# Optimization experiments

Measured on AMD Instinct MI355X. Metric: run time of the kernel, lower is better.

Reference implementation:

```python
import jax, jax.numpy as jnp
import numpy as np

T, B, IN, H, L = 1024, 128, 100, 200, 2


def _lstm_layer(x, h0, c0, W_ih, W_hh, b_ih, b_hh):
    # x: [T, B, in]; h0, c0: [B, H]; W_ih: [4H, in]; W_hh: [4H, H]
    # PyTorch gate order: i, f, g, o
    def step(carry, x_t):
        h, c = carry
        gates = x_t @ W_ih.T + b_ih + h @ W_hh.T + b_hh  # [B, 4H]
        i, f, g, o = jnp.split(gates, 4, axis=-1)
        i = jax.nn.sigmoid(i)
        f = jax.nn.sigmoid(f)
        g = jnp.tanh(g)
        o = jax.nn.sigmoid(o)
        c = f * c + i * g
        h = o * jnp.tanh(c)
        return (h, c), h

    (hT, cT), ys = jax.lax.scan(step, (h0, c0), x)
    return ys, hT, cT  # ys: [T, B, H]


def setup_inputs() -> dict:
    key = jax.random.key(0)
    ks = jax.random.split(key, 12)
    s = 1.0 / np.sqrt(H)  # PyTorch LSTM init scale
    return {
        "inp": jax.random.normal(ks[0], (T, B, IN), dtype=jnp.float32),
        "h0": jnp.zeros((L, B, H), dtype=jnp.float32),
        "c0": jnp.zeros((L, B, H), dtype=jnp.float32),
        "W_ih0": jax.random.uniform(ks[1], (4 * H, IN), jnp.float32, -s, s),
        "W_hh0": jax.random.uniform(ks[2], (4 * H, H), jnp.float32, -s, s),
        "b_ih0": jax.random.uniform(ks[3], (4 * H,), jnp.float32, -s, s),
        "b_hh0": jax.random.uniform(ks[4], (4 * H,), jnp.float32, -s, s),
        "W_ih1": jax.random.uniform(ks[5], (4 * H, H), jnp.float32, -s, s),
        "W_hh1": jax.random.uniform(ks[6], (4 * H, H), jnp.float32, -s, s),
        "b_ih1": jax.random.uniform(ks[7], (4 * H,), jnp.float32, -s, s),
        "b_hh1": jax.random.uniform(ks[8], (4 * H,), jnp.float32, -s, s),
        "fc_W": jax.random.uniform(ks[9], (IN, H), jnp.float32, -s, s),
        "fc_b": jax.random.uniform(ks[10], (IN,), jnp.float32, -s, s),
    }


def reference(inp, h0, c0, W_ih0, W_hh0, b_ih0, b_hh0, W_ih1, W_hh1, b_ih1, b_hh1, fc_W, fc_b):
    # 2-layer LSTM (eval mode: inter-layer dropout is identity) + linear head
    y0, h0T, c0T = _lstm_layer(inp, h0[0], c0[0], W_ih0, W_hh0, b_ih0, b_hh0)
    y1, h1T, c1T = _lstm_layer(y0, h0[1], c0[1], W_ih1, W_hh1, b_ih1, b_hh1)
    output = y1 @ fc_W.T + fc_b  # [T, B, num_classes]
    hn = jnp.stack([h0T, h1T], axis=0)  # [2, B, H]
    cn = jnp.stack([c0T, c1T], axis=0)
    return output, hn, cn
```

## Files before the change

### kernel.cpp

```cpp
#include <hip/hip_runtime.h>
#include <stdint.h>

#define T_ 1024
#define B_ 128
#define IN_ 100
#define H_ 200
#define RD 32
#define RDY 32

typedef unsigned short u16;
typedef unsigned long long u64;
typedef short bf16x8 __attribute__((ext_vector_type(8)));
typedef float f32x4  __attribute__((ext_vector_type(4)));

#define OFF_Y1    0u
#define OFF_Y0R   52428800u
#define OFF_PR0   55705600u
#define OFF_PR1A  68812800u
#define OFF_PR1B  81920000u
#define OFF_PACK  95027200u
#define OFF_CBF   96358400u
#define OFF_CH0   97525056u
#define OFF_CC0   97729856u
#define OFF_FLG   97934656u
#define WS_NEEDED 97938816u
#define FO_X0P  0u
#define FO_Y0P  512u
#define FO_W1A  1024u
#define FO_W1B  1536u
#define FO_WY0A 2048u
#define FO_WY0B 2560u
#define FO_CN0  3072u
#define FO_CN1  3584u
#define FO_DTF  4096u
#define PK_WHH0 0
#define PK_WHH1 179200
#define PK_WIH0 358400
#define PK_WIH1 460800

__device__ __forceinline__ float bf2f(u16 u) {
    union { uint32_t i; float f; } v; v.i = ((uint32_t)u) << 16; return v.f;
}
__device__ __forceinline__ u16 f2bf(float f) {
    union { uint32_t i; float f; } v; v.f = f;
    uint32_t x = v.i;
    x += 0x7fff + ((x >> 16) & 1);
    return (u16)(x >> 16);
}
__device__ __forceinline__ void agst2(float* p, float a, float b) {
    union { u64 u; float f[2]; } v; v.f[0] = a; v.f[1] = b;
    __hip_atomic_store((u64*)p, v.u, __ATOMIC_RELAXED, __HIP_MEMORY_SCOPE_AGENT);
}
__device__ __forceinline__ float2 agld2(const float* p) {
    union { u64 u; float f[2]; } v;
    v.u = __hip_atomic_load((u64*)p, __ATOMIC_RELAXED, __HIP_MEMORY_SCOPE_AGENT);
    return make_float2(v.f[0], v.f[1]);
}
__device__ __forceinline__ void agsti(int* p, int v) {
    __hip_atomic_store(p, v, __ATOMIC_RELAXED, __HIP_MEMORY_SCOPE_AGENT);
}
__device__ __forceinline__ void spin_ge(int* p, int val, int* budget) {
    while (__hip_atomic_load(p, __ATOMIC_RELAXED, __HIP_MEMORY_SCOPE_AGENT) < val) {
        __builtin_amdgcn_s_sleep(1);
        if (--(*budget) < 0) return;
    }
}
__device__ __forceinline__ float fsig(float x) {
    const float e = __expf(-x);
    return __builtin_amdgcn_rcpf(1.f + e);
}
__device__ __forceinline__ float ftanh(float x) {
    const float ax = __builtin_fabsf(x);
    const float e = __expf(-2.f * ax);
    const float r = (1.f - e) * __builtin_amdgcn_rcpf(1.f + e);
    return __builtin_copysignf(r, x);
}

__global__ void detect_kernel(const void* w, int* flag) {
    __shared__ int cnt;
    if (threadIdx.x == 0) cnt = 0;
    __syncthreads();
    const u16* p = (const u16*)w;
    int bad = 0;
    for (int e = 0; e < 16; ++e) {
        u16 u = p[threadIdx.x * 16 + e];
        int ex = (u >> 7) & 0xFF;
        float v = bf2f(u);
        float av = v < 0.f ? -v : v;
        if (ex == 0xFF || av > 0.5f) bad++;
    }
    atomicAdd(&cnt, bad);
    __syncthreads();
    if (threadIdx.x == 0) flag[0] = (cnt > 64) ? 1 : 0;
}

__global__ void prep_kernel(const void* Wih0, const void* Whh0,
                            const void* bih0, const void* bhh0,
                            const void* Wih1, const void* Whh1,
                            const void* bih1, const void* bhh1,
                            const void* fcW,  const void* fcb,
                            const void* h0,   const void* c0,
                            u16* cbf, float* ch0, float* cc0, const int* flag)
{
    const int isf32 = *flag;
    const int N = 685700;
    for (int idx = blockIdx.x * 256 + threadIdx.x; idx < N; idx += gridDim.x * 256) {
        const void* src; int e = idx; u16* du = nullptr; float* df = nullptr;
        if (e < 80000)                 { src = Wih0; du = cbf; }
        else if ((e -= 80000) < 160000){ src = Whh0; du = cbf + 80000; }
        else if ((e -= 160000) < 800)  { src = bih0; du = cbf + 240000; }
        else if ((e -= 800) < 800)     { src = bhh0; du = cbf + 240800; }
        else if ((e -= 800) < 160000)  { src = Wih1; du = cbf + 241600; }
        else if ((e -= 160000) < 160000){ src = Whh1; du = cbf + 401600; }
        else if ((e -= 160000) < 800)  { src = bih1; du = cbf + 561600; }
        else if ((e -= 800) < 800)     { src = bhh1; du = cbf + 562400; }
        else if ((e -= 800) < 20000)   { src = fcW;  du = cbf + 563200; }
        else if ((e -= 20000) < 100)   { src = fcb;  du = cbf + 583200; }
        else if ((e -= 100) < 51200)   { src = h0;   df = ch0; }
        else         { e -= 51200;       src = c0;   df = cc0; }
        float v = isf32 ? ((const float*)src)[e] : bf2f(((const u16*)src)[e]);
        if (du) du[e] = f2bf(v); else df[e] = v;
    }
}

__global__ void pack_kernel(const u16* __restrict__ cbf, u16* __restrict__ pw) {
    const int N = 665600;
    for (int idx = blockIdx.x * 256 + threadIdx.x; idx < N; idx += gridDim.x * 256) {
        int e = idx; const u16* src; int ld, koff, kmax, rel;
        if (e < 179200)                    { rel = e; src = cbf + 80000;  ld = 200; kmax = 200; koff = 0; }
        else if ((e -= 179200) < 179200)   { rel = e; src = cbf + 401600; ld = 200; kmax = 200; koff = 0; }
        else if ((e -= 179200) < 102400)   { rel = e; src = cbf + 0;      ld = 100; kmax = 100; koff = 0; }
        else { e -= 102400; const int kh = e / 102400; rel = e % 102400;
               src = cbf + 241600; ld = 200; kmax = 100; koff = kh * 100; }
        const int el = rel & 7, l = (rel >> 3) & 63, tile = rel >> 9;
        const int nt = tile % 50, kt = tile / 50;
        const int rp = nt * 16 + (l & 15), g = rp & 3, hc = rp >> 2;
        const int k = kt * 32 + ((l >> 4) << 3) + el;
        u16 v = 0;
        if (k < kmax) v = src[(g * 200 + hc) * ld + koff + k];
        pw[idx] = v;
    }
}

__launch_bounds__(512, 1)
__global__ void lstm_pipe(const void* __restrict__ inp, char* __restrict__ ws,
                          const int* __restrict__ flag, void* __restrict__ out)
{
    __shared__ __align__(16) u16 smem[67392];

    u16*   y1buf  = (u16*)(ws + OFF_Y1);
    float* y0ring = (float*)(ws + OFF_Y0R);
    float* pr0    = (float*)(ws + OFF_PR0);
    float* pr1a   = (float*)(ws + OFF_PR1A);
    float* pr1b   = (float*)(ws + OFF_PR1B);
    u16*   packs  = (u16*)(ws + OFF_PACK);
    const u16* cbf = (const u16*)(ws + OFF_CBF);
    const float* ch0 = (const float*)(ws + OFF_CH0);
    const float* cc0 = (const float*)(ws + OFF_CC0);

    const int isf32 = *flag;
    const int tid = threadIdx.x;
    const int bid = blockIdx.x;
    const int lane = tid & 63, wv = tid >> 6;
    const int lm = lane & 15, lq = lane >> 4;
    const int nslot = (wv < 2) ? 7 : 6;
    int budget = 1 << 22;

    if (bid < 16) {
        const int L = bid >> 3, i = bid & 7, b0 = i * 16;
        const int FI = i * 16;
        int* fx0p = (int*)(ws + OFF_FLG + FO_X0P) + FI;
        int* fw1a = (int*)(ws + OFF_FLG + FO_W1A) + FI;
        int* fw1b = (int*)(ws + OFF_FLG + FO_W1B) + FI;
        int* fwy0a= (int*)(ws + OFF_FLG + FO_WY0A) + FI;
        int* fwy0b= (int*)(ws + OFF_FLG + FO_WY0B) + FI;
        int* fy0p = (int*)(ws + OFF_FLG + FO_Y0P) + FI;
        int* fcn0 = (int*)(ws + OFF_FLG + FO_CN0) + FI;
        int* fcn1 = (int*)(ws + OFF_FLG + FO_CN1) + FI;

        u16* ldsB = smem;
        u16* hls  = smem + 31744;
        float* gls = (float*)(smem + 40192);
        const u16* packW = packs + (L ? PK_WHH1 : PK_WHH0);

        bf16x8 Bv[36];
        #pragma unroll
        for (int s = 0; s < 7; ++s) {
            const int nt = (s < 6) ? (wv + 8 * s) : (48 + wv);
            #pragma unroll
            for (int kt = 0; kt < 7; ++kt) {
                if (s < 5) {
                    Bv[s * 7 + kt] = *(const bf16x8*)(packW + ((size_t)(kt * 50 + nt) * 64 + lane) * 8);
                } else if (s == 5 && kt == 0) {
                    Bv[35] = *(const bf16x8*)(packW + ((size_t)(kt * 50 + nt) * 64 + lane) * 8);
                }
            }
        }
        for (int u = tid; u < 31744; u += 512) {
            const int eidx = u >> 9, off = u & 511;
            int kt, nt;
            if (eidx < 48) { kt = 1 + eidx % 6; nt = (eidx / 6) + 40; }
            else { const int e2 = eidx - 48; kt = e2 % 7; nt = 48 + e2 / 7; }
            ldsB[u] = packW[(size_t)(kt * 50 + nt) * 512 + off];
        }
        for (int u = tid; u < 2 * 16 * 264; u += 512) {
            const int pl = u / (16 * 264), m = (u / 264) % 16, k = u % 264;
            u16 v = 0;
            if (k < 200) {
                const float h = ch0[L * B_ * H_ + (b0 + m) * H_ + k];
                const u16 hi = f2bf(h);
                v = pl ? f2bf(h - bf2f(hi)) : hi;
            }
            hls[u] = v;
        }
        float c2[4][2];
        #pragma unroll
        for (int k4 = 0; k4 < 4; ++k4) {
            const int p = tid + 512 * k4;
            c2[k4][0] = 0.f; c2[k4][1] = 0.f;
            if (p < 1600) {
                const int m = p / 100, hc = (p % 100) * 2;
                c2[k4][0] = cc0[L * B_ * H_ + (b0 + m) * H_ + hc];
                c2[k4][1] = cc0[L * B_ * H_ + (b0 + m) * H_ + hc + 1];
            }
        }
        f32x4 acc[7];
        if (tid == 0) {
            if (L == 0) spin_ge(fx0p, 1, &budget);
            else        { spin_ge(fw1a, 1, &budget); spin_ge(fw1b, 1, &budget); }
        }
        __syncthreads();
        {
            const size_t roff = (size_t)(0 * 8 + i) * 12800;
            #pragma unroll
            for (int s = 0; s < 7; ++s) if (s < nslot) {
                const int nt = (s < 6) ? (wv + 8 * s) : (48 + wv);
                float* pa = ((L ? pr1a : pr0) + roff) + nt * 256 + lane * 4;
                const float2 a01 = agld2(pa);
                const float2 a23 = agld2(pa + 2);
                acc[s][0] = a01.x; acc[s][1] = a01.y;
                acc[s][2] = a23.x; acc[s][3] = a23.y;
                if (L) {
                    float* pb = (pr1b + roff) + nt * 256 + lane * 4;
                    const float2 b01 = agld2(pb);
                    const float2 b23 = agld2(pb + 2);
                    acc[s][0] += b01.x; acc[s][1] += b01.y;
                    acc[s][2] += b23.x; acc[s][3] += b23.y;
                }
            }
        }
        __syncthreads();

        for (int t = 0; t < T_; ++t) {
            #pragma unroll
            for (int kt = 0; kt < 7; ++kt) {
                const int ha = lm * 264 + kt * 32 + 8 * lq;
                const bf16x8 Ahi = *(const bf16x8*)(hls + ha);
                const bf16x8 Alo = *(const bf16x8*)(hls + 16 * 264 + ha);
                #pragma unroll
                for (int s = 0; s < 7; ++s) if (s < nslot) {
                    bf16x8 Bt;
                    if (s < 5)                 Bt = Bv[s * 7 + kt];
                    else if (s == 5 && kt == 0) Bt = Bv[35];
                    else {
                        const int eidx = (s == 5) ? (wv * 6 + kt - 1) : (48 + wv * 7 + kt);
                        Bt = *(const bf16x8*)(ldsB + eidx * 512 + lane * 8);
                    }
                    acc[s] = __builtin_amdgcn_mfma_f32_16x16x32_bf16(Ahi, Bt, acc[s], 0, 0, 0);
                    acc[s] = __builtin_amdgcn_mfma_f32_16x16x32_bf16(Alo, Bt, acc[s], 0, 0, 0);
                }
            }
            #pragma unroll
            for (int s = 0; s < 7; ++s) if (s < nslot) {
                const int nt = (s < 6) ? (wv + 8 * s) : (48 + wv);
                const int g = lm & 3, hc = nt * 4 + (lm >> 2);
                float* gp = gls + g * 3400 + hc * 17 + 4 * lq;
                gp[0] = acc[s][0]; gp[1] = acc[s][1]; gp[2] = acc[s][2]; gp[3] = acc[s][3];
            }
            __syncthreads();
            if ((t & 7) == 0) {
                if (tid == 0) {
                    int tgt = t + 9; if (tgt > T_) tgt = T_;
                    if (L == 0) {
                        spin_ge(fx0p, tgt, &budget);
                        spin_ge(fwy0a, t - 15, &budget);
                        spin_ge(fwy0b, t - 15, &budget);
                    } else {
                        spin_ge(fw1a, tgt, &budget);
                        spin_ge(fw1b, tgt, &budget);
                    }
                }
                __syncthreads();
            }
            if (t < T_ - 1) {
                const size_t roff = (size_t)(((t + 1) & (RD - 1)) * 8 + i) * 12800;
                #pragma unroll
                for (int s = 0; s < 7; ++s) if (s < nslot) {
                    const int nt = (s < 6) ? (wv + 8 * s) : (48 + wv);
                    float* pa = ((L ? pr1a : pr0) + roff) + nt * 256 + lane * 4;
                    const float2 a01 = agld2(pa);
                    const float2 a23 = agld2(pa + 2);
                    acc[s][0] = a01.x; acc[s][1] = a01.y;
                    acc[s][2] = a23.x; acc[s][3] = a23.y;
                    if (L) {
                        float* pb = (pr1b + roff) + nt * 256 + lane * 4;
                        const float2 b01 = agld2(pb);
                        const float2 b23 = agld2(pb + 2);
                        acc[s][0] += b01.x; acc[s][1] += b01.y;
                        acc[s][2] += b23.x; acc[s][3] += b23.y;
                    }
                }
            }
            #pragma unroll
            for (int k4 = 0; k4 < 4; ++k4) {
                const int p = tid + 512 * k4;
                if (p < 1600) {
                    const int m = p / 100, hc = (p % 100) * 2;
                    float ig0 = gls[hc * 17 + m],        ig1 = gls[(hc + 1) * 17 + m];
                    float fg0 = gls[3400 + hc * 17 + m], fg1 = gls[3400 + (hc + 1) * 17 + m];
                    float gg0 = gls[6800 + hc * 17 + m], gg1 = gls[6800 + (hc + 1) * 17 + m];
                    float og0 = gls[10200 + hc * 17 + m],og1 = gls[10200 + (hc + 1) * 17 + m];
                    ig0 = (ig0 == ig0) ? ig0 : 0.f;  ig1 = (ig1 == ig1) ? ig1 : 0.f;
                    fg0 = (fg0 == fg0) ? fg0 : 0.f;  fg1 = (fg1 == fg1) ? fg1 : 0.f;
                    gg0 = (gg0 == gg0) ? gg0 : 0.f;  gg1 = (gg1 == gg1) ? gg1 : 0.f;
                    og0 = (og0 == og0) ? og0 : 0.f;  og1 = (og1 == og1) ? og1 : 0.f;
                    ig0 = fsig(ig0); ig1 = fsig(ig1);
                    fg0 = fsig(fg0); fg1 = fsig(fg1);
                    og0 = fsig(og0); og1 = fsig(og1);
                    gg0 = ftanh(gg0); gg1 = ftanh(gg1);
                    c2[k4][0] = fg0 * c2[k4][0] + ig0 * gg0;
                    c2[k4][1] = fg1 * c2[k4][1] + ig1 * gg1;
                    const float h0v = og0 * ftanh(c2[k4][0]);
                    const float h1v = og1 * ftanh(c2[k4][1]);
                    const u16 hi0 = f2bf(h0v), hi1 = f2bf(h1v);
                    const u16 lo0 = f2bf(h0v - bf2f(hi0)), lo1 = f2bf(h1v - bf2f(hi1));
                    *(uint32_t*)(hls + m * 264 + hc) = (uint32_t)hi0 | ((uint32_t)hi1 << 16);
                    *(uint32_t*)(hls + (16 + m) * 264 + hc) = (uint32_t)lo0 | ((uint32_t)lo1 << 16);
                    if (L == 0) {
                        agst2(y0ring + ((size_t)(t & (RDY - 1)) * B_ + b0 + m) * H_ + hc, h0v, h1v);
                    } else {
                        *(uint32_t*)(y1buf + ((size_t)t * B_ + b0 + m) * H_ + hc)
                            = (uint32_t)hi0 | ((uint32_t)hi1 << 16);
                    }
                    if (t == T_ - 1) {
                        const size_t base = (size_t)T_ * B_ * IN_;
                        const size_t bb = (size_t)(b0 + m) * H_ + hc;
                        const size_t o1 = base + (size_t)L * B_ * H_ + bb;
                        const size_t o2 = base + 2 * (size_t)B_ * H_ + (size_t)L * B_ * H_ + bb;
                        if (isf32) {
                            ((float*)out)[o1] = h0v; ((float*)out)[o1 + 1] = h1v;
                            ((float*)out)[o2] = c2[k4][0]; ((float*)out)[o2 + 1] = c2[k4][1];
                        } else {
                            ((u16*)out)[o1] = hi0; ((u16*)out)[o1 + 1] = hi1;
                            ((u16*)out)[o2] = f2bf(c2[k4][0]); ((u16*)out)[o2 + 1] = f2bf(c2[k4][1]);
                        }
                    }
                }
            }
            __syncthreads();
            if (tid == 0) {
                if (L == 0) {
                    agsti(fy0p, t + 1);
                    if (((t + 1) & 7) == 0) agsti(fcn0, t + 1);
                } else {
                    if (((t + 1) & 7) == 0) agsti(fcn1, t + 1);
                }
            }
        }
    } else {
        const int isx0 = (bid < 24);
        const int i  = isx0 ? (bid - 16) : ((bid - 24) >> 1);
        const int kh = isx0 ? 0 : ((bid - 24) & 1);
        const int b0 = i * 16;
        const int FI = i * 16;
        int* fx0p = (int*)(ws + OFF_FLG + FO_X0P) + FI;
        int* fy0p = (int*)(ws + OFF_FLG + FO_Y0P) + FI;
        int* fw1  = (int*)(ws + OFF_FLG + (kh ? FO_W1B : FO_W1A)) + FI;
        int* fwy0 = (int*)(ws + OFF_FLG + (kh ? FO_WY0B : FO_WY0A)) + FI;
        int* fcons= (int*)(ws + OFF_FLG + (isx0 ? FO_CN0 : FO_CN1)) + FI;

        u16* xst = smem;
        const u16* packW = packs + (isx0 ? PK_WIH0 : (PK_WIH1 + kh * 102400));

        bf16x8 Bx[28];
        #pragma unroll
        for (int s = 0; s < 7; ++s) {
            const int nt = (s < 6) ? (wv + 8 * s) : (48 + wv);
            #pragma unroll
            for (int kt = 0; kt < 4; ++kt)
                if (s < nslot)
                    Bx[s * 4 + kt] = *(const bf16x8*)(packW + ((size_t)(kt * 50 + nt) * 64 + lane) * 8);
        }
        float bias[7];
        #pragma unroll
        for (int s = 0; s < 7; ++s) {
            bias[s] = 0.f;
            if (s < nslot && (isx0 || kh == 0)) {
                const int nt = (s < 6) ? (wv + 8 * s) : (48 + wv);
                const int rp = nt * 16 + lm, g = rp & 3, hc = rp >> 2, R = g * 200 + hc;
                bias[s] = isx0 ? (bf2f(cbf[240000 + R]) + bf2f(cbf[240800 + R]))
                               : (bf2f(cbf[561600 + R]) + bf2f(cbf[562400 + R]));
            }
        }
        for (int u = tid; u < 8704; u += 512) xst[u] = 0;

        float2 sreg[2];
        if (!isx0) { if (tid == 0) spin_ge(fy0p, 1, &budget); }
        __syncthreads();
        #pragma unroll
        for (int j = 0; j < 2; ++j) {
            const int u = tid + 512 * j;
            if (u < 800) {
                const int m = u / 50, k = (u % 50) * 2;
                if (isx0) {
                    const size_t gi = ((size_t)0 * B_ + b0 + m) * IN_ + k;
                    if (isf32) sreg[j] = *(const float2*)((const float*)inp + gi);
                    else { const uint32_t xv = *(const uint32_t*)((const u16*)inp + gi);
                           sreg[j] = make_float2(bf2f((u16)xv), bf2f((u16)(xv >> 16))); }
                } else {
                    sreg[j] = agld2(y0ring + ((size_t)0 * B_ + b0 + m) * H_ + kh * 100 + k);
                }
                const u16 h0 = f2bf(sreg[j].x), h1 = f2bf(sreg[j].y);
                *(uint32_t*)(xst + m * 136 + k) = (uint32_t)h0 | ((uint32_t)h1 << 16);
                *(uint32_t*)(xst + 2176 + m * 136 + k)
                    = (uint32_t)f2bf(sreg[j].x - bf2f(h0)) | ((uint32_t)f2bf(sreg[j].y - bf2f(h1)) << 16);
            }
        }
        __syncthreads();
        int cur = 0;

        for (int t = 0; t < T_; ++t) {
            if (t < T_ - 1) {
                if (tid == 0) {
                    if (isx0) {
                        if ((t & 7) == 0) spin_ge(fcons, t - 23, &budget);
                    } else {
                        spin_ge(fy0p, t + 2, &budget);
                        if ((t & 7) == 0) spin_ge(fcons, t - 23, &budget);
                    }
                }
                __syncthreads();
                #pragma unroll
                for (int j = 0; j < 2; ++j) {
                    const int u = tid + 512 * j;
                    if (u < 800) {
                        const int m = u / 50, k = (u % 50) * 2;
                        if (isx0) {
                            const size_t gi = ((size_t)(t + 1) * B_ + b0 + m) * IN_ + k;
                            if (isf32) sreg[j] = *(const float2*)((const float*)inp + gi);
                            else { const uint32_t xv = *(const uint32_t*)((const u16*)inp + gi);
                                   sreg[j] = make_float2(bf2f((u16)xv), bf2f((u16)(xv >> 16))); }
                        } else {
                            sreg[j] = agld2(y0ring + ((size_t)((t + 1) & (RDY - 1)) * B_ + b0 + m) * H_ + kh * 100 + k);
                        }
                    }
                }
            }
            f32x4 acc[7];
            #pragma unroll
            for (int s = 0; s < 7; ++s) {
                acc[s][0] = bias[s]; acc[s][1] = bias[s];
                acc[s][2] = bias[s]; acc[s][3] = bias[s];
            }
            #pragma unroll
            for (int kt = 0; kt < 4; ++kt) {
                const int xa = cur * 4352 + lm * 136 + kt * 32 + 8 * lq;
                const bf16x8 Ahi = *(const bf16x8*)(xst + xa);
                const bf16x8 Alo = *(const bf16x8*)(xst + 2176 + xa);
                #pragma unroll
                for (int s = 0; s < 7; ++s) if (s < nslot) {
                    acc[s] = __builtin_amdgcn_mfma_f32_16x16x32_bf16(Ahi, Bx[s * 4 + kt], acc[s], 0, 0, 0);
                    acc[s] = __builtin_amdgcn_mfma_f32_16x16x32_bf16(Alo, Bx[s * 4 + kt], acc[s], 0, 0, 0);
                }
            }
            float* ring = (isx0 ? pr0 : (kh ? pr1b : pr1a))
                        + (size_t)((t & (RD - 1)) * 8 + i) * 12800;
            #pragma unroll
            for (int s = 0; s < 7; ++s) if (s < nslot) {
                const int nt = (s < 6) ? (wv + 8 * s) : (48 + wv);
                float* pp = ring + nt * 256 + lane * 4;
                agst2(pp, acc[s][0], acc[s][1]);
                agst2(pp + 2, acc[s][2], acc[s][3]);
            }
            __syncthreads();
            if (tid == 0) {
                if (isx0) { if (((t + 1) & 3) == 0) agsti(fx0p, t + 1); }
                else      { agsti(fw1, t + 1); agsti(fwy0, t + 1); }
            }
            if (t < T_ - 1) {
                const int nb = (cur ^ 1) * 4352;
                #pragma unroll
                for (int j = 0; j < 2; ++j) {
                    const int u = tid + 512 * j;
                    if (u < 800) {
                        const int m = u / 50, k = (u % 50) * 2;
                        const u16 h0 = f2bf(sreg[j].x), h1 = f2bf(sreg[j].y);
                        *(uint32_t*)(xst + nb + m * 136 + k) = (uint32_t)h0 | ((uint32_t)h1 << 16);
                        *(uint32_t*)(xst + nb + 2176 + m * 136 + k)
                            = (uint32_t)f2bf(sreg[j].x - bf2f(h0)) | ((uint32_t)f2bf(sreg[j].y - bf2f(h1)) << 16);
                    }
                }
                __syncthreads();
                cur ^= 1;
            }
        }
    }
}

__launch_bounds__(256)
__global__ void fc_kernel(const u16* __restrict__ y1, const u16* __restrict__ cbf,
                          const int* __restrict__ flag, void* __restrict__ out)
{
    __shared__ float y1s[16 * 201];
    const int isf32 = *flag;
    const u16* fcW = cbf + 563200;
    const u16* fcb = cbf + 583200;
    const int tid = threadIdx.x;
    const int m0 = blockIdx.x * 16;
    for (int idx = tid; idx < 16 * 200; idx += 256) {
        int r = idx / 200, k = idx % 200;
        y1s[r * 201 + k] = bf2f(y1[(size_t)(m0 + r) * 200 + k]);
    }
    __syncthreads();
    const int r = tid & 15, ct = tid >> 4;
    float acc[7] = {0.f, 0.f, 0.f, 0.f, 0.f, 0.f, 0.f};
    for (int k = 0; k < 200; ++k) {
        const float x = y1s[r * 201 + k];
        #pragma unroll
        for (int qn = 0; qn < 7; ++qn) {
            int cc = ct + 16 * qn;
            if (cc < 100) acc[qn] = fmaf(x, bf2f(fcW[cc * 200 + k]), acc[qn]);
        }
    }
    #pragma unroll
    for (int qn = 0; qn < 7; ++qn) {
        int cc = ct + 16 * qn;
        if (cc < 100) {
            float v = acc[qn] + bf2f(fcb[cc]);
            v = (v == v) ? v : 0.f;
            const size_t oi = (size_t)(m0 + r) * 100 + cc;
            if (isf32) ((float*)out)[oi] = v;
            else       ((u16*)out)[oi] = f2bf(v);
        }
    }
}

extern "C" void kernel_launch(void* const* d_in, const int* in_sizes, int n_in,
                              void* d_out, int out_size, void* d_ws, size_t ws_size,
                              hipStream_t stream)
{
    const void* inp  = d_in[0];
    const void* h0   = d_in[1];
    const void* c0   = d_in[2];
    const void* Wih0 = d_in[3];
    const void* Whh0 = d_in[4];
    const void* bih0 = d_in[5];
    const void* bhh0 = d_in[6];
    const void* Wih1 = d_in[7];
    const void* Whh1 = d_in[8];
    const void* bih1 = d_in[9];
    const void* bhh1 = d_in[10];
    const void* fcW  = d_in[11];
    const void* fcb  = d_in[12];

    if (ws_size < WS_NEEDED) return;

    char* ws = (char*)d_ws;
    u16*   cbf  = (u16*)(ws + OFF_CBF);
    float* ch0  = (float*)(ws + OFF_CH0);
    float* cc0  = (float*)(ws + OFF_CC0);
    u16*   pw   = (u16*)(ws + OFF_PACK);
    int*   dflag= (int*)(ws + OFF_FLG + FO_DTF);
    u16*   y1buf= (u16*)(ws + OFF_Y1);

    hipMemsetAsync(ws + OFF_FLG, 0, 4160, stream);

    detect_kernel<<<1, 256, 0, stream>>>(Wih0, dflag);
    prep_kernel<<<512, 256, 0, stream>>>(Wih0, Whh0, bih0, bhh0,
                                         Wih1, Whh1, bih1, bhh1,
                                         fcW, fcb, h0, c0, cbf, ch0, cc0, dflag);
    pack_kernel<<<256, 256, 0, stream>>>(cbf, pw);
    lstm_pipe<<<40, 512, 0, stream>>>(inp, ws, dflag, d_out);
    fc_kernel<<<8192, 256, 0, stream>>>(y1buf, cbf, dflag, d_out);
}
```

Before: 6.453 ms.

## Compute LSTM cell in registers via DPP transposes and double-buffer hidden state

Gate pre-activations are no longer staged through an LDS gate buffer followed by a block-wide barrier. Each lane now uses two DPP quad permutes to gather the four gates (i, f, g, o) for one hidden unit straight from the MFMA accumulators and updates its cell state in registers. The hidden-state LDS buffer is double-buffered so the new h can be written while the current step's A operand is being read, which removes one __syncthreads per timestep and shrinks LDS use. The cost is more permute work, scalar stores in place of paired stores to the y0 ring and y1 buffer, and a layout whose correctness depends on the MFMA output mapping.

New measurement: 7.132 ms. 1.11x slower.

```diff
diff --git a/kernel.cpp b/kernel.cpp
--- a/kernel.cpp
+++ b/kernel.cpp
@@ -51,6 +51,9 @@
     union { u64 u; float f[2]; } v; v.f[0] = a; v.f[1] = b;
     __hip_atomic_store((u64*)p, v.u, __ATOMIC_RELAXED, __HIP_MEMORY_SCOPE_AGENT);
 }
+__device__ __forceinline__ void agst1(float* p, float a) {
+    __hip_atomic_store(p, a, __ATOMIC_RELAXED, __HIP_MEMORY_SCOPE_AGENT);
+}
 __device__ __forceinline__ float2 agld2(const float* p) {
     union { u64 u; float f[2]; } v;
     v.u = __hip_atomic_load((u64*)p, __ATOMIC_RELAXED, __HIP_MEMORY_SCOPE_AGENT);
@@ -75,6 +78,15 @@
     const float r = (1.f - e) * __builtin_amdgcn_rcpf(1.f + e);
     return __builtin_copysignf(r, x);
 }
+template<int CTRL>
+__device__ __forceinline__ float qperm(float x) {
+    union { float f; int i; } u, r;
+    u.f = x;
+    r.i = __builtin_amdgcn_update_dpp(0, u.i, CTRL, 0xF, 0xF, true);
+    return r.f;
+}
+#define QP_XOR1 177
+#define QP_XOR2 78
 
 __global__ void detect_kernel(const void* w, int* flag) {
     __shared__ int cnt;
@@ -146,7 +158,7 @@
 __global__ void lstm_pipe(const void* __restrict__ inp, char* __restrict__ ws,
                           const int* __restrict__ flag, void* __restrict__ out)
 {
-    __shared__ __align__(16) u16 smem[67392];
+    __shared__ __align__(16) u16 smem[48640];
 
     u16*   y1buf  = (u16*)(ws + OFF_Y1);
     float* y0ring = (float*)(ws + OFF_Y0R);
@@ -180,8 +192,10 @@
 
         u16* ldsB = smem;
         u16* hls  = smem + 31744;
-        float* gls = (float*)(smem + 40192);
         const u16* packW = packs + (L ? PK_WHH1 : PK_WHH0);
+
+        const int fm  = 4 * lq + (lane & 3);
+        const int fa  = (lane >> 2) & 3;
 
         bf16x8 Bv[36];
         #pragma unroll
@@ -203,8 +217,8 @@
             else { const int e2 = eidx - 48; kt = e2 % 7; nt = 48 + e2 / 7; }
             ldsB[u] = packW[(size_t)(kt * 50 + nt) * 512 + off];
         }
-        for (int u = tid; u < 2 * 16 * 264; u += 512) {
-            const int pl = u / (16 * 264), m = (u / 264) % 16, k = u % 264;
+        for (int u = tid; u < 8448; u += 512) {
+            const int pl = u / 4224, m = (u / 264) % 16, k = u % 264;
             u16 v = 0;
             if (k < 200) {
                 const float h = ch0[L * B_ * H_ + (b0 + m) * H_ + k];
@@ -212,16 +226,15 @@
                 v = pl ? f2bf(h - bf2f(hi)) : hi;
             }
             hls[u] = v;
-        }
-        float c2[4][2];
+            hls[8448 + u] = 0;
+        }
+        float c2s[7];
         #pragma unroll
-        for (int k4 = 0; k4 < 4; ++k4) {
-            const int p = tid + 512 * k4;
-            c2[k4][0] = 0.f; c2[k4][1] = 0.f;
-            if (p < 1600) {
-                const int m = p / 100, hc = (p % 100) * 2;
-                c2[k4][0] = cc0[L * B_ * H_ + (b0 + m) * H_ + hc];
-                c2[k4][1] = cc0[L * B_ * H_ + (b0 + m) * H_ + hc + 1];
+        for (int s = 0; s < 7; ++s) {
+            c2s[s] = 0.f;
+            if (s < nslot) {
+                const int nt = (s < 6) ? (wv + 8 * s) : (48 + wv);
+                c2s[s] = cc0[L * B_ * H_ + (b0 + fm) * H_ + nt * 4 + fa];
             }
         }
         f32x4 acc[7];
@@ -252,11 +265,12 @@
         __syncthreads();
 
         for (int t = 0; t < T_; ++t) {
+            const int rdb = (t & 1) * 8448;
             #pragma unroll
             for (int kt = 0; kt < 7; ++kt) {
-                const int ha = lm * 264 + kt * 32 + 8 * lq;
+                const int ha = rdb + lm * 264 + kt * 32 + 8 * lq;
                 const bf16x8 Ahi = *(const bf16x8*)(hls + ha);
-                const bf16x8 Alo = *(const bf16x8*)(hls + 16 * 264 + ha);
+                const bf16x8 Alo = *(const bf16x8*)(hls + 4224 + ha);
                 #pragma unroll
                 for (int s = 0; s < 7; ++s) if (s < nslot) {
                     bf16x8 Bt;
@@ -270,14 +284,6 @@
                     acc[s] = __builtin_amdgcn_mfma_f32_16x16x32_bf16(Alo, Bt, acc[s], 0, 0, 0);
                 }
             }
-            #pragma unroll
-            for (int s = 0; s < 7; ++s) if (s < nslot) {
-                const int nt = (s < 6) ? (wv + 8 * s) : (48 + wv);
-                const int g = lm & 3, hc = nt * 4 + (lm >> 2);
-                float* gp = gls + g * 3400 + hc * 17 + 4 * lq;
-                gp[0] = acc[s][0]; gp[1] = acc[s][1]; gp[2] = acc[s][2]; gp[3] = acc[s][3];
-            }
-            __syncthreads();
             if ((t & 7) == 0) {
                 if (tid == 0) {
                     int tgt = t + 9; if (tgt > T_) tgt = T_;
@@ -292,6 +298,7 @@
                 }
                 __syncthreads();
             }
+            f32x4 pf[7];
             if (t < T_ - 1) {
                 const size_t roff = (size_t)(((t + 1) & (RD - 1)) * 8 + i) * 12800;
                 #pragma unroll
@@ -300,62 +307,75 @@
                     float* pa = ((L ? pr1a : pr0) + roff) + nt * 256 + lane * 4;
                     const float2 a01 = agld2(pa);
                     const float2 a23 = agld2(pa + 2);
-                    acc[s][0] = a01.x; acc[s][1] = a01.y;
-                    acc[s][2] = a23.x; acc[s][3] = a23.y;
+                    pf[s][0] = a01.x; pf[s][1] = a01.y;
+                    pf[s][2] = a23.x; pf[s][3] = a23.y;
                     if (L) {
                         float* pb = (pr1b + roff) + nt * 256 + lane * 4;
                         const float2 b01 = agld2(pb);
                         const float2 b23 = agld2(pb + 2);
-                        acc[s][0] += b01.x; acc[s][1] += b01.y;
-                        acc[s][2] += b23.x; acc[s][3] += b23.y;
+                        pf[s][0] += b01.x; pf[s][1] += b01.y;
+                        pf[s][2] += b23.x; pf[s][3] += b23.y;
                     }
                 }
             }
-            #pragma unroll
-            for (int k4 = 0; k4 < 4; ++k4) {
-                const int p = tid + 512 * k4;
-                if (p < 1600) {
-                    const int m = p / 100, hc = (p % 100) * 2;
-                    float ig0 = gls[hc * 17 + m],        ig1 = gls[(hc + 1) * 17 + m];
-                    float fg0 = gls[3400 + hc * 17 + m], fg1 = gls[3400 + (hc + 1) * 17 + m];
-                    float gg0 = gls[6800 + hc * 17 + m], gg1 = gls[6800 + (hc + 1) * 17 + m];
-                    float og0 = gls[10200 + hc * 17 + m],og1 = gls[10200 + (hc + 1) * 17 + m];
-                    ig0 = (ig0 == ig0) ? ig0 : 0.f;  ig1 = (ig1 == ig1) ? ig1 : 0.f;
-                    fg0 = (fg0 == fg0) ? fg0 : 0.f;  fg1 = (fg1 == fg1) ? fg1 : 0.f;
-                    gg0 = (gg0 == gg0) ? gg0 : 0.f;  gg1 = (gg1 == gg1) ? gg1 : 0.f;
-                    og0 = (og0 == og0) ? og0 : 0.f;  og1 = (og1 == og1) ? og1 : 0.f;
-                    ig0 = fsig(ig0); ig1 = fsig(ig1);
-                    fg0 = fsig(fg0); fg1 = fsig(fg1);
-                    og0 = fsig(og0); og1 = fsig(og1);
-                    gg0 = ftanh(gg0); gg1 = ftanh(gg1);
-                    c2[k4][0] = fg0 * c2[k4][0] + ig0 * gg0;
-                    c2[k4][1] = fg1 * c2[k4][1] + ig1 * gg1;
-                    const float h0v = og0 * ftanh(c2[k4][0]);
-                    const float h1v = og1 * ftanh(c2[k4][1]);
-                    const u16 hi0 = f2bf(h0v), hi1 = f2bf(h1v);
-                    const u16 lo0 = f2bf(h0v - bf2f(hi0)), lo1 = f2bf(h1v - bf2f(hi1));
-                    *(uint32_t*)(hls + m * 264 + hc) = (uint32_t)hi0 | ((uint32_t)hi1 << 16);
-                    *(uint32_t*)(hls + (16 + m) * 264 + hc) = (uint32_t)lo0 | ((uint32_t)lo1 << 16);
-                    if (L == 0) {
-                        agst2(y0ring + ((size_t)(t & (RDY - 1)) * B_ + b0 + m) * H_ + hc, h0v, h1v);
-                    } else {
-                        *(uint32_t*)(y1buf + ((size_t)t * B_ + b0 + m) * H_ + hc)
-                            = (uint32_t)hi0 | ((uint32_t)hi1 << 16);
-                    }
-                    if (t == T_ - 1) {
-                        const size_t base = (size_t)T_ * B_ * IN_;
-                        const size_t bb = (size_t)(b0 + m) * H_ + hc;
-                        const size_t o1 = base + (size_t)L * B_ * H_ + bb;
-                        const size_t o2 = base + 2 * (size_t)B_ * H_ + (size_t)L * B_ * H_ + bb;
-                        if (isf32) {
-                            ((float*)out)[o1] = h0v; ((float*)out)[o1 + 1] = h1v;
-                            ((float*)out)[o2] = c2[k4][0]; ((float*)out)[o2 + 1] = c2[k4][1];
-                        } else {
-                            ((u16*)out)[o1] = hi0; ((u16*)out)[o1 + 1] = hi1;
-                            ((u16*)out)[o2] = f2bf(c2[k4][0]); ((u16*)out)[o2 + 1] = f2bf(c2[k4][1]);
-                        }
-                    }
-                }
+            const int wrb = ((t & 1) ^ 1) * 8448;
+            #pragma unroll
+            for (int s = 0; s < 7; ++s) if (s < nslot) {
+                f32x4 v = acc[s];
+                {
+                    const float t0 = qperm<QP_XOR1>(v[1]);
+                    const float t1 = qperm<QP_XOR1>(v[0]);
+                    const float t2 = qperm<QP_XOR1>(v[3]);
+                    const float t3 = qperm<QP_XOR1>(v[2]);
+                    const bool b1 = ((lane & 1) == 0);
+                    v[0] = b1 ? v[0] : t0;
+                    v[1] = b1 ? t1 : v[1];
+                    v[2] = b1 ? v[2] : t2;
+                    v[3] = b1 ? t3 : v[3];
+                }
+                {
+                    const float s0 = qperm<QP_XOR2>(v[2]);
+                    const float s1 = qperm<QP_XOR2>(v[3]);
+                    const float s2 = qperm<QP_XOR2>(v[0]);
+                    const float s3 = qperm<QP_XOR2>(v[1]);
+                    const bool b2 = ((lane & 2) == 0);
+                    v[0] = b2 ? v[0] : s0;
+                    v[1] = b2 ? v[1] : s1;
+                    v[2] = b2 ? s2 : v[2];
+                    v[3] = b2 ? s3 : v[3];
+                }
+                float ig = v[0], fg = v[1], gg = v[2], og = v[3];
+                ig = (ig == ig) ? ig : 0.f;
+                fg = (fg == fg) ? fg : 0.f;
+                gg = (gg == gg) ? gg : 0.f;
+                og = (og == og) ? og : 0.f;
+                ig = fsig(ig); fg = fsig(fg); og = fsig(og); gg = ftanh(gg);
+                float c = fg * c2s[s] + ig * gg;
+                c2s[s] = c;
+                const float h = og * ftanh(c);
+                const int nt = (s < 6) ? (wv + 8 * s) : (48 + wv);
+                const int hc = nt * 4 + fa;
+                const u16 hi = f2bf(h);
+                const u16 lo = f2bf(h - bf2f(hi));
+                hls[wrb + fm * 264 + hc] = hi;
+                hls[wrb + 4224 + fm * 264 + hc] = lo;
+                if (L == 0) {
+                    agst1(y0ring + ((size_t)(t & (RDY - 1)) * B_ + b0 + fm) * H_ + hc, h);
+                } else {
+                    y1buf[((size_t)t * B_ + b0 + fm) * H_ + hc] = hi;
+                }
+                if (t == T_ - 1) {
+                    const size_t base = (size_t)T_ * B_ * IN_;
+                    const size_t bb = (size_t)(b0 + fm) * H_ + hc;
+                    const size_t o1 = base + (size_t)L * B_ * H_ + bb;
+                    const size_t o2 = base + 2 * (size_t)B_ * H_ + (size_t)L * B_ * H_ + bb;
+                    if (isf32) { ((float*)out)[o1] = h; ((float*)out)[o2] = c; }
+                    else       { ((u16*)out)[o1] = hi; ((u16*)out)[o2] = f2bf(c); }
+                }
+            }
+            if (t < T_ - 1) {
+                #pragma unroll
+                for (int s = 0; s < 7; ++s) if (s < nslot) acc[s] = pf[s];
             }
             __syncthreads();
             if (tid == 0) {
```
